# Optimization experiments

Measured on AMD Instinct MI355X. Metric: run time of the kernel, lower is better.

The kernel has to match this reference:

```python
import jax, jax.numpy as jnp
import numpy as np

N = 50000   # nodes
E = 800000  # edges (avg degree 16)
H = 256     # hidden_dim
OUT = 256   # out_dim


def _leaky(x, slope=0.01):
    return jnp.where(x >= 0, x, slope * x)


def _mlp3(x, W1, b1, W2, b2, W3, b3):
    # MLP(hidden, hidden/2, hidden/2, hidden) with LeakyReLU(0.01) between layers
    x = _leaky(x @ W1 + b1)
    x = _leaky(x @ W2 + b2)
    return x @ W3 + b3


def setup_inputs() -> dict:
    key = jax.random.key(0)
    ks = jax.random.split(key, 16)
    Hh = H // 2

    def w(k, i, o):
        return (jax.random.normal(k, (i, o), jnp.float32) / np.float32(np.sqrt(i)))

    return {
        'h': jax.random.normal(ks[0], (N, H), jnp.float32),
        'src': jax.random.randint(ks[1], (E,), 0, N, dtype=jnp.int32),
        'dst': jax.random.randint(ks[2], (E,), 0, N, dtype=jnp.int32),
        'r': jax.random.randint(ks[3], (E,), 0, 2, dtype=jnp.int32),
        'inv': jax.random.randint(ks[4], (N,), 0, 2, dtype=jnp.int32),
        'inv_W1': w(ks[5], H, Hh), 'inv_b1': jnp.zeros((Hh,), jnp.float32),
        'inv_W2': w(ks[6], Hh, Hh), 'inv_b2': jnp.zeros((Hh,), jnp.float32),
        'inv_W3': w(ks[7], Hh, H), 'inv_b3': jnp.zeros((H,), jnp.float32),
        'and_W1': w(ks[8], H, Hh), 'and_b1': jnp.zeros((Hh,), jnp.float32),
        'and_W2': w(ks[9], Hh, Hh), 'and_b2': jnp.zeros((Hh,), jnp.float32),
        'and_W3': w(ks[10], Hh, H), 'and_b3': jnp.zeros((H,), jnp.float32),
        'proj_W1': w(ks[11], H, H), 'proj_b1': jnp.zeros((H,), jnp.float32),
        'proj_W2': w(ks[12], H, OUT), 'proj_b2': jnp.zeros((OUT,), jnp.float32),
    }


def reference(h, src, dst, r, inv,
              inv_W1, inv_b1, inv_W2, inv_b2, inv_W3, inv_b3,
              and_W1, and_b1, and_W2, and_b2, and_W3, and_b3,
              proj_W1, proj_b1, proj_W2, proj_b2):
    # edge_msg: gather src features, apply func_inv on edges with r == 1
    msg = h[src]  # [E, H]
    msg = jnp.where((r == 1)[:, None],
                    _mlp3(msg, inv_W1, inv_b1, inv_W2, inv_b2, inv_W3, inv_b3),
                    msg)
    # fn.mean('m', 'neigh'): mean over incoming edges per destination node
    sums = jax.ops.segment_sum(msg, dst, num_segments=N)          # [N, H]
    cnt = jax.ops.segment_sum(jnp.ones((E,), msg.dtype), dst, num_segments=N)
    neigh = sums / jnp.maximum(cnt, 1.0)[:, None]
    # apply_nodes_func: func_and, then func_inv where inv flag set
    res = _mlp3(neigh, and_W1, and_b1, and_W2, and_b2, and_W3, and_b3)
    res = jnp.where((inv == 1)[:, None],
                    _mlp3(res, inv_W1, inv_b1, inv_W2, inv_b2, inv_W3, inv_b3),
                    res)
    # proj_head: MLP(H, H, OUT) with negative_slope=0 (i.e. ReLU)
    out = jax.nn.relu(res @ proj_W1 + proj_b1) @ proj_W2 + proj_b2
    return out
```

## Files before the change

### kernel.cpp

```cpp
#include <hip/hip_runtime.h>

typedef _Float16 f16_t;
typedef f16_t f16x2 __attribute__((ext_vector_type(2)));
typedef f16_t f16x4 __attribute__((ext_vector_type(4)));
typedef f16_t f16x8 __attribute__((ext_vector_type(8)));
typedef float f32x4 __attribute__((ext_vector_type(4)));
typedef float f32x16 __attribute__((ext_vector_type(16)));

#define MFMA16H(a, b, c) __builtin_amdgcn_mfma_f32_16x16x32_f16(a, b, c, 0, 0, 0)
#define MFMA32H(a, b, c) __builtin_amdgcn_mfma_f32_32x32x16_f16(a, b, c, 0, 0, 0)

__device__ __forceinline__ float leaky01(float v) { return v >= 0.f ? v : 0.01f * v; }

__device__ __forceinline__ void acc_f16x4(float& s0, float& s1, float& s2, float& s3,
                                          f16x4 v)
{
#if __has_builtin(__builtin_amdgcn_fdot2)
    const f16x2 K10 = (f16x2){(f16_t)1.0f, (f16_t)0.0f};
    const f16x2 K01 = (f16x2){(f16_t)0.0f, (f16_t)1.0f};
    f16x2 lo = (f16x2){v.x, v.y};
    f16x2 hi = (f16x2){v.z, v.w};
    s0 = __builtin_amdgcn_fdot2(lo, K10, s0, false);
    s1 = __builtin_amdgcn_fdot2(lo, K01, s1, false);
    s2 = __builtin_amdgcn_fdot2(hi, K10, s2, false);
    s3 = __builtin_amdgcn_fdot2(hi, K01, s3, false);
#else
    s0 += (float)v.x; s1 += (float)v.y; s2 += (float)v.z; s3 += (float)v.w;
#endif
}

#define OFF_IW1 0
#define OFF_IW2 32768
#define OFF_IW3 49152
#define OFF_AW1 81920
#define OFF_AW2 114688
#define OFF_AW3 131072
#define OFF_PW1 163840
#define OFF_PW2 229376
#define OFF_M3  294912
#define WP_TOTAL 311296

template<int KD, int NC>
__device__ __forceinline__ void gemm16(
    const f16_t* __restrict__ a, int sa, const f16_t* __restrict__ B,
    int cb, int qd, int ln, f32x4 (&acc)[4])
{
#pragma unroll
    for (int rt = 0; rt < 4; ++rt) acc[rt] = (f32x4){0.f, 0.f, 0.f, 0.f};
#pragma unroll
    for (int k0 = 0; k0 < KD; k0 += 32) {
        int ka = k0 + qd * 8;
        f16x8 b = *(const f16x8*)(B + ((size_t)((k0 >> 5) * 4 + qd) * NC + cb + ln) * 8);
        f16x8 a0 = *(const f16x8*)&a[ln * sa + ka];
        f16x8 a1 = *(const f16x8*)&a[(16 + ln) * sa + ka];
        f16x8 a2 = *(const f16x8*)&a[(32 + ln) * sa + ka];
        f16x8 a3 = *(const f16x8*)&a[(48 + ln) * sa + ka];
        acc[0] = MFMA16H(a0, b, acc[0]);
        acc[1] = MFMA16H(a1, b, acc[1]);
        acc[2] = MFMA16H(a2, b, acc[2]);
        acc[3] = MFMA16H(a3, b, acc[3]);
    }
}

template<int KD, int NC>
__device__ __forceinline__ void gemm32(
    const f16_t* __restrict__ a, int sa, const f16_t* __restrict__ B,
    int cb, int l31, int kh, f32x16 &o0, f32x16 &o1)
{
    f32x16 c0, c1;
#pragma unroll
    for (int i = 0; i < 16; ++i) { c0[i] = 0.f; c1[i] = 0.f; }
    const int ar0 = l31 * sa + kh * 8;
    const int ar1 = (32 + l31) * sa + kh * 8;
    const int bcol = cb + l31;
#pragma unroll
    for (int kc = 0; kc < KD; kc += 32) {
        f16x8 b0 = *(const f16x8*)(B + ((size_t)((kc >> 3) + kh) * NC + bcol) * 8);
        f16x8 b1 = *(const f16x8*)(B + ((size_t)((kc >> 3) + 2 + kh) * NC + bcol) * 8);
        f16x8 a00 = *(const f16x8*)&a[ar0 + kc];
        f16x8 a01 = *(const f16x8*)&a[ar0 + kc + 16];
        f16x8 a10 = *(const f16x8*)&a[ar1 + kc];
        f16x8 a11 = *(const f16x8*)&a[ar1 + kc + 16];
        c0 = MFMA32H(a00, b0, c0);
        c1 = MFMA32H(a10, b0, c1);
        c0 = MFMA32H(a01, b1, c0);
        c1 = MFMA32H(a11, b1, c1);
    }
    o0 = c0; o1 = c1;
}

template<int ACT>
__device__ __forceinline__ void epi16(
    f32x4 (&acc)[4], const float* __restrict__ bias,
    int cb, int qd, int ln, f16_t* d, int stride)
{
    int col = cb + ln;
    float bb = bias[col];
#pragma unroll
    for (int rt = 0; rt < 4; ++rt)
#pragma unroll
        for (int r = 0; r < 4; ++r) {
            float v = acc[rt][r] + bb;
            if (ACT == 1) v = leaky01(v);
            else if (ACT == 2) v = fmaxf(v, 0.f);
            d[(rt * 16 + qd * 4 + r) * stride + col] = (f16_t)v;
        }
}

template<int ACT>
__device__ __forceinline__ void epi32(
    const f32x16 &a0, const f32x16 &a1, const float* __restrict__ bias,
    int cb, int l31, int kh, f16_t* d, int stride)
{
    int col = cb + l31;
    float bb = bias[col];
#pragma unroll
    for (int r = 0; r < 16; ++r) {
        float v0 = a0[r] + bb;
        float v1 = a1[r] + bb;
        if (ACT == 1) { v0 = leaky01(v0); v1 = leaky01(v1); }
        else if (ACT == 2) { v0 = fmaxf(v0, 0.f); v1 = fmaxf(v1, 0.f); }
        int row = (r & 3) + 8 * (r >> 2) + 4 * kh;
        d[row * stride + col] = (f16_t)v0;
        d[(32 + row) * stride + col] = (f16_t)v1;
    }
}

__global__ __launch_bounds__(512, 4) void kernelA(
    const float* __restrict__ h, f16_t* __restrict__ zbuf,
    const f16_t* __restrict__ wp, const float* __restrict__ ib1,
    const float* __restrict__ ib2, const float* __restrict__ c3f, int M,
    int tiles, const int* __restrict__ dstE, int* __restrict__ cnt, int E)
{
    __shared__ f16_t X[64][264];
    __shared__ f16_t Y[64][136];

    const int tid = threadIdx.x;

    if ((int)blockIdx.x >= tiles) {
        int e = (blockIdx.x - tiles) * 512 + tid;
        if (e < E) atomicAdd(&cnt[dstE[e]], 1);
        return;
    }

    const int row0 = blockIdx.x * 64;
    const int lane = tid & 63;
    const int wv = tid >> 6;
    const int qd = lane >> 4;
    const int ln = lane & 15;
    const int cb = wv * 16;
    const int l31 = lane & 31;
    const int kh = lane >> 5;

    {
        const float4* src4 = (const float4*)(h + (size_t)row0 * 256);
#pragma unroll
        for (int i = 0; i < 8; ++i) {
            int q = i * 512 + tid;
            int row = q >> 6;
            int kc = (q & 63) * 4;
            float4 v = make_float4(0.f, 0.f, 0.f, 0.f);
            if (row0 + row < M) v = src4[q];
            *(f16x4*)&X[row][kc] = (f16x4){(f16_t)v.x, (f16_t)v.y, (f16_t)v.z, (f16_t)v.w};
        }
    }
    __syncthreads();

    {
        const bool isz = wv < 4;
        const int cb32 = (wv & 3) * 32;
        const f16_t* Bw = wp + (isz ? OFF_AW1 : OFF_IW1);
        f32x16 z0, z1;
        gemm32<256, 128>(&X[0][0], 264, Bw, cb32, l31, kh, z0, z1);
        __syncthreads();
        int col = cb32 + l31;
        if (isz) {
#pragma unroll
            for (int r = 0; r < 16; ++r) {
                int lrow = (r & 3) + 8 * (r >> 2) + 4 * kh;
                X[lrow][128 + col] = (f16_t)z0[r];
                X[32 + lrow][128 + col] = (f16_t)z1[r];
            }
        } else {
            float bb = ib1[col];
#pragma unroll
            for (int r = 0; r < 16; ++r) {
                int lrow = (r & 3) + 8 * (r >> 2) + 4 * kh;
                Y[lrow][col] = (f16_t)leaky01(z0[r] + bb);
                Y[32 + lrow][col] = (f16_t)leaky01(z1[r] + bb);
            }
        }
    }
    __syncthreads();

    f32x4 a4[4];

    gemm16<128, 128>(&Y[0][0], 136, wp + OFF_IW2, cb, qd, ln, a4);
    epi16<1>(a4, ib2, cb, qd, ln, &X[0][0], 264);
    __syncthreads();

    gemm16<128, 128>(&X[0][0], 264, wp + OFF_M3, cb, qd, ln, a4);
    {
        int col = cb + ln;
        float bb = c3f[col];
#pragma unroll
        for (int rt = 0; rt < 4; ++rt)
#pragma unroll
            for (int r = 0; r < 4; ++r)
                Y[rt * 16 + qd * 4 + r][col] = (f16_t)(a4[rt][r] + bb);
    }
    __syncthreads();

#pragma unroll
    for (int i = 0; i < 4; ++i) {
        int q = i * 512 + tid;
        int node = q >> 5;
        int seg = q & 31;
        int row = row0 + node;
        if (row < M) {
            f16x8 v = (seg < 16) ? *(const f16x8*)&X[node][128 + seg * 8]
                                 : *(const f16x8*)&Y[node][(seg - 16) * 8];
            *(f16x8*)&zbuf[(size_t)row * 256 + seg * 8] = v;
        }
    }
}

__global__ __launch_bounds__(512, 4) void kernelB(
    const f16_t* __restrict__ zbuf, const int* __restrict__ ridx,
    const int* __restrict__ offs, const int* __restrict__ cnt,
    const float* __restrict__ ab1, const int* __restrict__ invf,
    float* __restrict__ out, const f16_t* __restrict__ wp,
    const float* __restrict__ ab2, const float* __restrict__ ab3,
    const float* __restrict__ ib1, const float* __restrict__ ib2,
    const float* __restrict__ ib3, const float* __restrict__ pb1,
    const float* __restrict__ pb2, int M)
{
    __shared__ f16_t C[64][264];
    __shared__ f16_t A[64][136];
    __shared__ int sflag[64];

    const int tid = threadIdx.x;
    const int row0 = blockIdx.x * 64;
    const int lane = tid & 63;
    const int wv = tid >> 6;
    const int qd = lane >> 4;
    const int ln = lane & 15;
    const int cb2 = wv * 16;
    const int l31 = lane & 31;
    const int kh = lane >> 5;
    const int cb32 = wv * 32;

    const int hw = tid >> 5;
    const int hl = tid & 31;
    const int hbase = lane & 32;
    const f16x4* zp4 = (const f16x4*)zbuf;

#pragma unroll
    for (int pass = 0; pass < 4; ++pass) {
        int nl = pass * 16 + hw;
        int row = row0 + nl;
        float s0 = 0.f, s1 = 0.f, s2 = 0.f, s3 = 0.f;
        int c = 0;
        if (row < M) {
            int beg = offs[row];
            c = cnt[row];
            for (int base = 0; base < c; base += 32) {
                int rem = c - base; if (rem > 32) rem = 32;
                int myr = (hl < rem) ? ridx[beg + base + hl] : 0;
                int j = 0;
                for (; j + 16 <= rem; j += 16) {
                    f16x4 v[16];
#pragma unroll
                    for (int i = 0; i < 16; ++i) {
                        int rr = __shfl(myr, hbase + j + i);
                        v[i] = zp4[(size_t)rr * 32 + hl];
                    }
#pragma unroll
                    for (int i = 0; i < 16; ++i)
                        acc_f16x4(s0, s1, s2, s3, v[i]);
                }
                for (; j + 8 <= rem; j += 8) {
                    f16x4 v[8];
#pragma unroll
                    for (int i = 0; i < 8; ++i) {
                        int rr = __shfl(myr, hbase + j + i);
                        v[i] = zp4[(size_t)rr * 32 + hl];
                    }
#pragma unroll
                    for (int i = 0; i < 8; ++i)
                        acc_f16x4(s0, s1, s2, s3, v[i]);
                }
                for (; j < rem; ++j) {
                    int rr = __shfl(myr, hbase + j);
                    f16x4 vv = zp4[(size_t)rr * 32 + hl];
                    acc_f16x4(s0, s1, s2, s3, vv);
                }
            }
        }
        float invc = 1.0f / fmaxf((float)c, 1.0f);
        float4 bv = *(const float4*)&ab1[hl * 4];
        float m0 = leaky01(s0 * invc + bv.x);
        float m1 = leaky01(s1 * invc + bv.y);
        float m2 = leaky01(s2 * invc + bv.z);
        float m3 = leaky01(s3 * invc + bv.w);
        *(f16x4*)&A[nl][hl * 4] = (f16x4){(f16_t)m0, (f16_t)m1, (f16_t)m2, (f16_t)m3};
    }
    if (tid < 64) {
        int rr = row0 + tid;
        sflag[tid] = (rr < M) ? invf[rr] : 0;
    }
    __syncthreads();

    f32x4 a4[4];
    f32x16 c0, c1;

    gemm16<128, 128>(&A[0][0], 136, wp + OFF_AW2, cb2, qd, ln, a4);
    __syncthreads();
    epi16<1>(a4, ab2, cb2, qd, ln, &A[0][0], 136);
    __syncthreads();

    gemm32<128, 256>(&A[0][0], 136, wp + OFF_AW3, cb32, l31, kh, c0, c1);
    epi32<0>(c0, c1, ab3, cb32, l31, kh, &C[0][0], 264);
    __syncthreads();

    gemm16<256, 128>(&C[0][0], 264, wp + OFF_IW1, cb2, qd, ln, a4);
    epi16<1>(a4, ib1, cb2, qd, ln, &A[0][0], 136);
    __syncthreads();

    gemm16<128, 128>(&A[0][0], 136, wp + OFF_IW2, cb2, qd, ln, a4);
    __syncthreads();
    epi16<1>(a4, ib2, cb2, qd, ln, &A[0][0], 136);
    __syncthreads();

    gemm32<128, 256>(&A[0][0], 136, wp + OFF_IW3, cb32, l31, kh, c0, c1);
    {
        int col = cb32 + l31;
        float bb = ib3[col];
#pragma unroll
        for (int r = 0; r < 16; ++r) {
            int lrow = (r & 3) + 8 * (r >> 2) + 4 * kh;
            if (sflag[lrow] == 1) C[lrow][col] = (f16_t)(c0[r] + bb);
            if (sflag[32 + lrow] == 1) C[32 + lrow][col] = (f16_t)(c1[r] + bb);
        }
    }
    __syncthreads();

    gemm32<256, 256>(&C[0][0], 264, wp + OFF_PW1, cb32, l31, kh, c0, c1);
    __syncthreads();
    epi32<2>(c0, c1, pb1, cb32, l31, kh, &C[0][0], 264);
    __syncthreads();

    gemm32<256, 256>(&C[0][0], 264, wp + OFF_PW2, cb32, l31, kh, c0, c1);
    {
        int col = cb32 + l31;
        float bb = pb2[col];
#pragma unroll
        for (int r = 0; r < 16; ++r) {
            int lrow = (r & 3) + 8 * (r >> 2) + 4 * kh;
            int row = row0 + lrow;
            if (row < M) out[(size_t)row * 256 + col] = c0[r] + bb;
            row += 32;
            if (row < M) out[(size_t)row * 256 + col] = c1[r] + bb;
        }
    }
}

__global__ void pack_mc3(const float* s0, const float* s1, const float* s2,
                         const float* s3, const float* s4, const float* s5,
                         const float* s6, const float* s7,
                         const float* __restrict__ ib3, f16_t* dst,
                         float* __restrict__ c3f)
{
    int m = blockIdx.y;
    int bx = blockIdx.x;
    if (m == 8) {
        if (bx < 64) {
            int idx = bx * 256 + threadIdx.x;
            int k = idx >> 7, j = idx & 127;
            float s = 0.f;
            for (int t = 0; t < 256; ++t) s += s2[k * 256 + t] * s3[t * 128 + j];
            int p = ((k >> 3) * 128 + j) * 8 + (k & 7);
            dst[OFF_M3 + p] = (f16_t)s;
        } else if (bx == 64) {
            int j = threadIdx.x;
            if (j < 128) {
                float s = 0.f;
                for (int t = 0; t < 256; ++t) s += ib3[t] * s3[t * 128 + j];
                c3f[j] = s;
            }
        }
        return;
    }
    const float* srcs[8] = {s0, s1, s2, s3, s4, s5, s6, s7};
    const int lgN[8] = {7, 7, 8, 7, 7, 8, 8, 8};
    const int sz[8]  = {32768, 16384, 32768, 32768, 16384, 32768, 65536, 65536};
    const int off[8] = {OFF_IW1, OFF_IW2, OFF_IW3, OFF_AW1, OFF_AW2, OFF_AW3,
                        OFF_PW1, OFF_PW2};
    int idx = bx * blockDim.x + threadIdx.x;
    if (idx >= sz[m]) return;
    int lg = lgN[m];
    int Nc = 1 << lg;
    int k = idx >> lg;
    int n = idx & (Nc - 1);
    int p = ((k >> 3) * Nc + n) * 8 + (k & 7);
    dst[off[m] + p] = (f16_t)srcs[m][idx];
}

__global__ void scan1(const int* __restrict__ cnt, int* __restrict__ offs,
                      int* __restrict__ bsum, int Nn)
{
    __shared__ int s[256];
    int tid = threadIdx.x;
    int g = blockIdx.x * 256 + tid;
    int v = (g < Nn) ? cnt[g] : 0;
    s[tid] = v;
    __syncthreads();
    for (int off = 1; off < 256; off <<= 1) {
        int u = (tid >= off) ? s[tid - off] : 0;
        __syncthreads();
        s[tid] += u;
        __syncthreads();
    }
    if (g < Nn) offs[g] = s[tid] - v;
    if (tid == 255) bsum[blockIdx.x] = s[255];
}

__global__ void scan3b(int* __restrict__ offs, const int* __restrict__ bsum,
                       int* __restrict__ cursor, int Nn, int NB)
{
    __shared__ int s[256];
    int tid = threadIdx.x;
    int bid = blockIdx.x;
    int v = (tid < NB) ? bsum[tid] : 0;
    s[tid] = v;
    __syncthreads();
    for (int off = 1; off < 256; off <<= 1) {
        int u = (tid >= off) ? s[tid - off] : 0;
        __syncthreads();
        s[tid] += u;
        __syncthreads();
    }
    int base = (bid > 0) ? s[bid - 1] : 0;
    int g = bid * 256 + tid;
    if (g < Nn) {
        int o = offs[g] + base;
        offs[g] = o;
        cursor[g] = o;
    }
}

__global__ void scan2(int* __restrict__ bsum, int NB)
{
    if (threadIdx.x == 0) {
        int run = 0;
        for (int i = 0; i < NB; ++i) { int v = bsum[i]; bsum[i] = run; run += v; }
    }
}

__global__ void scan3(int* __restrict__ offs, const int* __restrict__ bsum,
                      int* __restrict__ cursor, int Nn)
{
    int g = blockIdx.x * 256 + threadIdx.x;
    if (g < Nn) {
        int o = offs[g] + bsum[blockIdx.x];
        offs[g] = o;
        cursor[g] = o;
    }
}

__global__ void fill_kernel(const int* __restrict__ dst, const int* __restrict__ src,
                            const int* __restrict__ r, int* __restrict__ cursor,
                            int* __restrict__ ridx, int E)
{
    int e = blockIdx.x * blockDim.x + threadIdx.x;
    if (e < E) {
        int p = atomicAdd(&cursor[dst[e]], 1);
        ridx[p] = src[e] * 2 + r[e];
    }
}

extern "C" void kernel_launch(void* const* d_in, const int* in_sizes, int n_in,
                              void* d_out, int out_size, void* d_ws, size_t ws_size,
                              hipStream_t stream)
{
    const float* h   = (const float*)d_in[0];
    const int* src   = (const int*)d_in[1];
    const int* dst   = (const int*)d_in[2];
    const int* r     = (const int*)d_in[3];
    const int* inv   = (const int*)d_in[4];
    const float* iW1 = (const float*)d_in[5];
    const float* ib1 = (const float*)d_in[6];
    const float* iW2 = (const float*)d_in[7];
    const float* ib2 = (const float*)d_in[8];
    const float* iW3 = (const float*)d_in[9];
    const float* ib3 = (const float*)d_in[10];
    const float* aW1 = (const float*)d_in[11];
    const float* ab1 = (const float*)d_in[12];
    const float* aW2 = (const float*)d_in[13];
    const float* ab2 = (const float*)d_in[14];
    const float* aW3 = (const float*)d_in[15];
    const float* ab3 = (const float*)d_in[16];
    const float* pW1 = (const float*)d_in[17];
    const float* pb1 = (const float*)d_in[18];
    const float* pW2 = (const float*)d_in[19];
    const float* pb2 = (const float*)d_in[20];

    const int N = in_sizes[0] / 256;
    const int E = in_sizes[1];
    float* out = (float*)d_out;

    f16_t* zbuf = (f16_t*)d_ws;
    int* cnt    = (int*)(zbuf + (size_t)2 * N * 128);
    int* offs   = cnt + N;
    int* cursor = offs + N;
    int* bsum   = cursor + N;
    int* ridx   = bsum + 256;
    f16_t* wp   = (f16_t*)(ridx + E);
    float* c3f  = (float*)(wp + WP_TOTAL);

    (void)hipMemsetAsync(cnt, 0, (size_t)N * sizeof(int), stream);

    pack_mc3<<<dim3(256, 9), 256, 0, stream>>>(iW1, iW2, iW3, aW1, aW2, aW3,
                                               pW1, pW2, ib3, wp, c3f);

    const int tiles = (N + 63) / 64;
    const int EB = (E + 511) / 512;
    const int NB = (N + 255) / 256;

    kernelA<<<tiles + EB, 512, 0, stream>>>(h, zbuf, wp, ib1, ib2, c3f, N,
                                            tiles, dst, cnt, E);

    scan1<<<NB, 256, 0, stream>>>(cnt, offs, bsum, N);
    if (NB <= 256) {
        scan3b<<<NB, 256, 0, stream>>>(offs, bsum, cursor, N, NB);
    } else {
        scan2<<<1, 1, 0, stream>>>(bsum, NB);
        scan3<<<NB, 256, 0, stream>>>(offs, bsum, cursor, N);
    }
    fill_kernel<<<(E + 255) / 256, 256, 0, stream>>>(dst, src, r, cursor, ridx, E);

    kernelB<<<tiles, 512, 0, stream>>>(zbuf, ridx, offs, cnt, ab1, inv, out, wp,
                                       ab2, ab3, ib1, ib2, ib3, pb1, pb2, N);
}
```

Baseline: 339.2 us.

## Halve node tile to 32 rows and split edge counting into its own kernel

Node tile size in both fused MLP kernels drops from 64 to 32 rows. The GEMM helpers are reworked to compute a single 32-row slab, which halves accumulator registers and LDS per block, and launch bounds are raised to 8 blocks per CU for higher occupancy. Edge degree counting moves out of kernelA into a separate count_kernel launch. In exchange, each weight fragment loaded from global memory is reused across fewer rows, and there is an extra kernel launch.

```diff
diff --git a/kernel.cpp b/kernel.cpp
--- a/kernel.cpp
+++ b/kernel.cpp
@@ -43,61 +43,52 @@
 template<int KD, int NC>
 __device__ __forceinline__ void gemm16(
     const f16_t* __restrict__ a, int sa, const f16_t* __restrict__ B,
-    int cb, int qd, int ln, f32x4 (&acc)[4])
-{
-#pragma unroll
-    for (int rt = 0; rt < 4; ++rt) acc[rt] = (f32x4){0.f, 0.f, 0.f, 0.f};
+    int cb, int qd, int ln, f32x4 (&acc)[2])
+{
+    acc[0] = (f32x4){0.f, 0.f, 0.f, 0.f};
+    acc[1] = acc[0];
 #pragma unroll
     for (int k0 = 0; k0 < KD; k0 += 32) {
         int ka = k0 + qd * 8;
         f16x8 b = *(const f16x8*)(B + ((size_t)((k0 >> 5) * 4 + qd) * NC + cb + ln) * 8);
         f16x8 a0 = *(const f16x8*)&a[ln * sa + ka];
         f16x8 a1 = *(const f16x8*)&a[(16 + ln) * sa + ka];
-        f16x8 a2 = *(const f16x8*)&a[(32 + ln) * sa + ka];
-        f16x8 a3 = *(const f16x8*)&a[(48 + ln) * sa + ka];
         acc[0] = MFMA16H(a0, b, acc[0]);
         acc[1] = MFMA16H(a1, b, acc[1]);
-        acc[2] = MFMA16H(a2, b, acc[2]);
-        acc[3] = MFMA16H(a3, b, acc[3]);
     }
 }
 
 template<int KD, int NC>
 __device__ __forceinline__ void gemm32(
     const f16_t* __restrict__ a, int sa, const f16_t* __restrict__ B,
-    int cb, int l31, int kh, f32x16 &o0, f32x16 &o1)
-{
-    f32x16 c0, c1;
-#pragma unroll
-    for (int i = 0; i < 16; ++i) { c0[i] = 0.f; c1[i] = 0.f; }
-    const int ar0 = l31 * sa + kh * 8;
-    const int ar1 = (32 + l31) * sa + kh * 8;
+    int cb, int l31, int kh, f32x16 &o)
+{
+    f32x16 c;
+#pragma unroll
+    for (int i = 0; i < 16; ++i) c[i] = 0.f;
+    const int ar = l31 * sa + kh * 8;
     const int bcol = cb + l31;
 #pragma unroll
     for (int kc = 0; kc < KD; kc += 32) {
         f16x8 b0 = *(const f16x8*)(B + ((size_t)((kc >> 3) + kh) * NC + bcol) * 8);
         f16x8 b1 = *(const f16x8*)(B + ((size_t)((kc >> 3) + 2 + kh) * NC + bcol) * 8);
-        f16x8 a00 = *(const f16x8*)&a[ar0 + kc];
-        f16x8 a01 = *(const f16x8*)&a[ar0 + kc + 16];
-        f16x8 a10 = *(const f16x8*)&a[ar1 + kc];
-        f16x8 a11 = *(const f16x8*)&a[ar1 + kc + 16];
-        c0 = MFMA32H(a00, b0, c0);
-        c1 = MFMA32H(a10, b0, c1);
-        c0 = MFMA32H(a01, b1, c0);
-        c1 = MFMA32H(a11, b1, c1);
-    }
-    o0 = c0; o1 = c1;
+        f16x8 a0 = *(const f16x8*)&a[ar + kc];
+        f16x8 a1 = *(const f16x8*)&a[ar + kc + 16];
+        c = MFMA32H(a0, b0, c);
+        c = MFMA32H(a1, b1, c);
+    }
+    o = c;
 }
 
 template<int ACT>
 __device__ __forceinline__ void epi16(
-    f32x4 (&acc)[4], const float* __restrict__ bias,
+    f32x4 (&acc)[2], const float* __restrict__ bias,
     int cb, int qd, int ln, f16_t* d, int stride)
 {
     int col = cb + ln;
     float bb = bias[col];
 #pragma unroll
-    for (int rt = 0; rt < 4; ++rt)
+    for (int rt = 0; rt < 2; ++rt)
 #pragma unroll
         for (int r = 0; r < 4; ++r) {
             float v = acc[rt][r] + bb;
@@ -109,41 +100,38 @@
 
 template<int ACT>
 __device__ __forceinline__ void epi32(
-    const f32x16 &a0, const f32x16 &a1, const float* __restrict__ bias,
+    const f32x16 &a0, const float* __restrict__ bias,
     int cb, int l31, int kh, f16_t* d, int stride)
 {
     int col = cb + l31;
     float bb = bias[col];
 #pragma unroll
     for (int r = 0; r < 16; ++r) {
-        float v0 = a0[r] + bb;
-        float v1 = a1[r] + bb;
-        if (ACT == 1) { v0 = leaky01(v0); v1 = leaky01(v1); }
-        else if (ACT == 2) { v0 = fmaxf(v0, 0.f); v1 = fmaxf(v1, 0.f); }
+        float v = a0[r] + bb;
+        if (ACT == 1) v = leaky01(v);
+        else if (ACT == 2) v = fmaxf(v, 0.f);
         int row = (r & 3) + 8 * (r >> 2) + 4 * kh;
-        d[row * stride + col] = (f16_t)v0;
-        d[(32 + row) * stride + col] = (f16_t)v1;
-    }
-}
-
-__global__ __launch_bounds__(512, 4) void kernelA(
+        d[row * stride + col] = (f16_t)v;
+    }
+}
+
+__global__ void count_kernel(const int* __restrict__ dstE, int* __restrict__ cnt,
+                             int E)
+{
+    int e = blockIdx.x * blockDim.x + threadIdx.x;
+    if (e < E) atomicAdd(&cnt[dstE[e]], 1);
+}
+
+__global__ __launch_bounds__(512, 8) void kernelA(
     const float* __restrict__ h, f16_t* __restrict__ zbuf,
     const f16_t* __restrict__ wp, const float* __restrict__ ib1,
-    const float* __restrict__ ib2, const float* __restrict__ c3f, int M,
-    int tiles, const int* __restrict__ dstE, int* __restrict__ cnt, int E)
-{
-    __shared__ f16_t X[64][264];
-    __shared__ f16_t Y[64][136];
+    const float* __restrict__ ib2, const float* __restrict__ c3f, int M)
+{
+    __shared__ f16_t X[32][264];
+    __shared__ f16_t Y[32][136];
 
     const int tid = threadIdx.x;
-
-    if ((int)blockIdx.x >= tiles) {
-        int e = (blockIdx.x - tiles) * 512 + tid;
-        if (e < E) atomicAdd(&cnt[dstE[e]], 1);
-        return;
-    }
-
-    const int row0 = blockIdx.x * 64;
+    const int row0 = blockIdx.x * 32;
     const int lane = tid & 63;
     const int wv = tid >> 6;
     const int qd = lane >> 4;
@@ -155,7 +143,7 @@
     {
         const float4* src4 = (const float4*)(h + (size_t)row0 * 256);
 #pragma unroll
-        for (int i = 0; i < 8; ++i) {
+        for (int i = 0; i < 4; ++i) {
             int q = i * 512 + tid;
             int row = q >> 6;
             int kc = (q & 63) * 4;
@@ -170,30 +158,28 @@
         const bool isz = wv < 4;
         const int cb32 = (wv & 3) * 32;
         const f16_t* Bw = wp + (isz ? OFF_AW1 : OFF_IW1);
-        f32x16 z0, z1;
-        gemm32<256, 128>(&X[0][0], 264, Bw, cb32, l31, kh, z0, z1);
+        f32x16 z;
+        gemm32<256, 128>(&X[0][0], 264, Bw, cb32, l31, kh, z);
         __syncthreads();
         int col = cb32 + l31;
         if (isz) {
 #pragma unroll
             for (int r = 0; r < 16; ++r) {
                 int lrow = (r & 3) + 8 * (r >> 2) + 4 * kh;
-                X[lrow][128 + col] = (f16_t)z0[r];
-                X[32 + lrow][128 + col] = (f16_t)z1[r];
+                X[lrow][128 + col] = (f16_t)z[r];
             }
         } else {
             float bb = ib1[col];
 #pragma unroll
             for (int r = 0; r < 16; ++r) {
                 int lrow = (r & 3) + 8 * (r >> 2) + 4 * kh;
-                Y[lrow][col] = (f16_t)leaky01(z0[r] + bb);
-                Y[32 + lrow][col] = (f16_t)leaky01(z1[r] + bb);
+                Y[lrow][col] = (f16_t)leaky01(z[r] + bb);
             }
         }
     }
     __syncthreads();
 
-    f32x4 a4[4];
+    f32x4 a4[2];
 
     gemm16<128, 128>(&Y[0][0], 136, wp + OFF_IW2, cb, qd, ln, a4);
     epi16<1>(a4, ib2, cb, qd, ln, &X[0][0], 264);
@@ -204,7 +190,7 @@
         int col = cb + ln;
         float bb = c3f[col];
 #pragma unroll
-        for (int rt = 0; rt < 4; ++rt)
+        for (int rt = 0; rt < 2; ++rt)
 #pragma unroll
             for (int r = 0; r < 4; ++r)
                 Y[rt * 16 + qd * 4 + r][col] = (f16_t)(a4[rt][r] + bb);
@@ -212,7 +198,7 @@
     __syncthreads();
 
 #pragma unroll
-    for (int i = 0; i < 4; ++i) {
+    for (int i = 0; i < 2; ++i) {
         int q = i * 512 + tid;
         int node = q >> 5;
         int seg = q & 31;
@@ -225,7 +211,7 @@
     }
 }
 
-__global__ __launch_bounds__(512, 4) void kernelB(
+__global__ __launch_bounds__(512, 8) void kernelB(
     const f16_t* __restrict__ zbuf, const int* __restrict__ ridx,
     const int* __restrict__ offs, const int* __restrict__ cnt,
     const float* __restrict__ ab1, const int* __restrict__ invf,
@@ -235,12 +221,12 @@
     const float* __restrict__ ib3, const float* __restrict__ pb1,
     const float* __restrict__ pb2, int M)
 {
-    __shared__ f16_t C[64][264];
-    __shared__ f16_t A[64][136];
-    __shared__ int sflag[64];
+    __shared__ f16_t C[32][264];
+    __shared__ f16_t A[32][136];
+    __shared__ int sflag[32];
 
     const int tid = threadIdx.x;
-    const int row0 = blockIdx.x * 64;
+    const int row0 = blockIdx.x * 32;
     const int lane = tid & 63;
     const int wv = tid >> 6;
     const int qd = lane >> 4;
@@ -256,7 +242,7 @@
     const f16x4* zp4 = (const f16x4*)zbuf;
 
 #pragma unroll
-    for (int pass = 0; pass < 4; ++pass) {
+    for (int pass = 0; pass < 2; ++pass) {
         int nl = pass * 16 + hw;
         int row = row0 + nl;
         float s0 = 0.f, s1 = 0.f, s2 = 0.f, s3 = 0.f;
@@ -305,22 +291,22 @@
         float m3 = leaky01(s3 * invc + bv.w);
         *(f16x4*)&A[nl][hl * 4] = (f16x4){(f16_t)m0, (f16_t)m1, (f16_t)m2, (f16_t)m3};
     }
-    if (tid < 64) {
+    if (tid < 32) {
         int rr = row0 + tid;
         sflag[tid] = (rr < M) ? invf[rr] : 0;
     }
     __syncthreads();
 
-    f32x4 a4[4];
-    f32x16 c0, c1;
+    f32x4 a4[2];
+    f32x16 c32;
 
     gemm16<128, 128>(&A[0][0], 136, wp + OFF_AW2, cb2, qd, ln, a4);
     __syncthreads();
     epi16<1>(a4, ab2, cb2, qd, ln, &A[0][0], 136);
     __syncthreads();
 
-    gemm32<128, 256>(&A[0][0], 136, wp + OFF_AW3, cb32, l31, kh, c0, c1);
-    epi32<0>(c0, c1, ab3, cb32, l31, kh, &C[0][0], 264);
+    gemm32<128, 256>(&A[0][0], 136, wp + OFF_AW3, cb32, l31, kh, c32);
+    epi32<0>(c32, ab3, cb32, l31, kh, &C[0][0], 264);
     __syncthreads();
 
     gemm16<256, 128>(&C[0][0], 264, wp + OFF_IW1, cb2, qd, ln, a4);
@@ -332,25 +318,24 @@
     epi16<1>(a4, ib2, cb2, qd, ln, &A[0][0], 136);
     __syncthreads();
 
-    gemm32<128, 256>(&A[0][0], 136, wp + OFF_IW3, cb32, l31, kh, c0, c1);
+    gemm32<128, 256>(&A[0][0], 136, wp + OFF_IW3, cb32, l31, kh, c32);
     {
         int col = cb32 + l31;
         float bb = ib3[col];
 #pragma unroll
         for (int r = 0; r < 16; ++r) {
             int lrow = (r & 3) + 8 * (r >> 2) + 4 * kh;
-            if (sflag[lrow] == 1) C[lrow][col] = (f16_t)(c0[r] + bb);
-            if (sflag[32 + lrow] == 1) C[32 + lrow][col] = (f16_t)(c1[r] + bb);
-        }
-    }
-    __syncthreads();
-
-    gemm32<256, 256>(&C[0][0], 264, wp + OFF_PW1, cb32, l31, kh, c0, c1);
-    __syncthreads();
-    epi32<2>(c0, c1, pb1, cb32, l31, kh, &C[0][0], 264);
-    __syncthreads();
-
-    gemm32<256, 256>(&C[0][0], 264, wp + OFF_PW2, cb32, l31, kh, c0, c1);
+            if (sflag[lrow] == 1) C[lrow][col] = (f16_t)(c32[r] + bb);
+        }
+    }
+    __syncthreads();
+
+    gemm32<256, 256>(&C[0][0], 264, wp + OFF_PW1, cb32, l31, kh, c32);
+    __syncthreads();
+    epi32<2>(c32, pb1, cb32, l31, kh, &C[0][0], 264);
+    __syncthreads();
+
+    gemm32<256, 256>(&C[0][0], 264, wp + OFF_PW2, cb32, l31, kh, c32);
     {
         int col = cb32 + l31;
         float bb = pb2[col];
@@ -358,9 +343,7 @@
         for (int r = 0; r < 16; ++r) {
             int lrow = (r & 3) + 8 * (r >> 2) + 4 * kh;
             int row = row0 + lrow;
-            if (row < M) out[(size_t)row * 256 + col] = c0[r] + bb;
-            row += 32;
-            if (row < M) out[(size_t)row * 256 + col] = c1[r] + bb;
+            if (row < M) out[(size_t)row * 256 + col] = c32[r] + bb;
         }
     }
 }
@@ -523,12 +506,13 @@
     pack_mc3<<<dim3(256, 9), 256, 0, stream>>>(iW1, iW2, iW3, aW1, aW2, aW3,
                                                pW1, pW2, ib3, wp, c3f);
 
-    const int tiles = (N + 63) / 64;
+    const int tiles = (N + 31) / 32;
     const int EB = (E + 511) / 512;
     const int NB = (N + 255) / 256;
 
-    kernelA<<<tiles + EB, 512, 0, stream>>>(h, zbuf, wp, ib1, ib2, c3f, N,
-                                            tiles, dst, cnt, E);
+    count_kernel<<<EB, 512, 0, stream>>>(dst, cnt, E);
+
+    kernelA<<<tiles, 512, 0, stream>>>(h, zbuf, wp, ib1, ib2, c3f, N);
 
     scan1<<<NB, 256, 0, stream>>>(cnt, offs, bsum, N);
     if (NB <= 256) {
```

After: 330.2 us. -2.7%, faster.
